# Kernel optimization log

Measured on AMD Instinct MI355X. Metric: run time of the kernel, lower is better.

Reference implementation:

```python
import jax, jax.numpy as jnp
import numpy as np

N, D_IN, D_ATTN = 8192, 48, 8


def setup_inputs() -> dict:
    key = jax.random.key(0)
    ks = jax.random.split(key, 9)
    s = 1.0 / np.sqrt(D_IN)
    return {
        "x": jax.random.normal(ks[0], (N, D_IN), jnp.float32),
        "Kw": jax.random.normal(ks[1], (D_IN, D_ATTN), jnp.float32) * s,
        "Kb": jax.random.normal(ks[2], (D_ATTN,), jnp.float32) * s,
        "Qw": jax.random.normal(ks[3], (D_IN, D_ATTN), jnp.float32) * s,
        "Qb": jax.random.normal(ks[4], (D_ATTN,), jnp.float32) * s,
        "Vw": jax.random.normal(ks[5], (D_IN, D_ATTN), jnp.float32) * s,
        "Vb": jax.random.normal(ks[6], (D_ATTN,), jnp.float32) * s,
        "Zw": jax.random.normal(ks[7], (D_ATTN, D_IN), jnp.float32) * (1.0 / np.sqrt(D_ATTN)),
        "Zb": jax.random.normal(ks[8], (D_IN,), jnp.float32) * (1.0 / np.sqrt(D_ATTN)),
    }


def reference(x, Kw, Kb, Qw, Qb, Vw, Vb, Zw, Zb):
    # Tiny QKV projections: [N,48] -> [N,8]
    Xk = x @ Kw + Kb
    Xq = x @ Qw + Qb
    Xv = x @ Vw + Vb
    # Attention over the batch/row dimension: [N,8]@[8,N] -> [N,N]
    scale = jnp.sqrt(jnp.asarray(D_ATTN, jnp.float32))
    AM = jax.nn.softmax(Xk @ Xq.T / scale, axis=1)  # torch F.softmax 2D default dim=1
    Z = AM @ Xv                                      # [N,8]
    return x + (Z @ Zw + Zb)                         # residual + output proj [N,48]
```

## Files before the change

kernel.cpp:

```cpp
#include <hip/hip_runtime.h>


#define QV_OFF   32768
#define BMAX_OFF 98304
#define PART_OFF 98560

typedef _Float16 f16x2 __attribute__((ext_vector_type(2)));

union HU { unsigned u; f16x2 h; };

static __device__ __forceinline__ unsigned pku(float a, float b) {
    auto v = __builtin_amdgcn_cvt_pkrtz(a, b);
    union { decltype(v) v2; unsigned u; } t;
    t.v2 = v;
    return t.u;
}
static __device__ __forceinline__ f16x2 asH2(unsigned u) {
    HU t; t.u = u; return t.h;
}
static __device__ __forceinline__ float fdot2(f16x2 a, f16x2 b, float c) {
#if __has_builtin(__builtin_amdgcn_fdot2)
    return __builtin_amdgcn_fdot2(a, b, c, false);
#else
    return fmaf((float)a.x, (float)b.x, fmaf((float)a.y, (float)b.y, c));
#endif
}

__global__ __launch_bounds__(256) void proj_kernel(
    const float* __restrict__ x,
    const float* __restrict__ Kw, const float* __restrict__ Kb,
    const float* __restrict__ Qw, const float* __restrict__ Qb,
    const float* __restrict__ Vw, const float* __restrict__ Vb,
    unsigned* __restrict__ Xksf16, unsigned* __restrict__ QV,
    float* __restrict__ bmax)
{
    __shared__ float xs[32 * 49];
    __shared__ float wAll[3 * 388];
    __shared__ float bs[24];
    __shared__ float outv[32][25];
    const int tid = threadIdx.x;
    const int r0 = blockIdx.x * 32;

    for (int i = tid; i < 1536; i += 256) {
        int r = i / 48, c = i - r * 48;
        xs[r * 49 + c] = x[r0 * 48 + i];
    }
    for (int i = tid; i < 384; i += 256) {
        wAll[i]       = Kw[i];
        wAll[388 + i] = Qw[i];
        wAll[776 + i] = Vw[i];
    }
    if (tid < 8)       bs[tid] = Kb[tid];
    else if (tid < 16) bs[tid] = Qb[tid - 8];
    else if (tid < 24) bs[tid] = Vb[tid - 16];
    __syncthreads();

    const int rl = tid >> 3;
    const int g  = tid & 7;
    const int c0 = 3 * g;
    const float* xr = &xs[rl * 49];
    const float* w0 = &wAll[((c0 + 0) >> 3) * 388 + ((c0 + 0) & 7)];
    const float* w1 = &wAll[((c0 + 1) >> 3) * 388 + ((c0 + 1) & 7)];
    const float* w2 = &wAll[((c0 + 2) >> 3) * 388 + ((c0 + 2) & 7)];
    float a0 = bs[c0], a1 = bs[c0 + 1], a2 = bs[c0 + 2];
    #pragma unroll
    for (int k = 0; k < 48; k++) {
        const float xv = xr[k];
        a0 = fmaf(xv, w0[k * 8], a0);
        a1 = fmaf(xv, w1[k * 8], a1);
        a2 = fmaf(xv, w2[k * 8], a2);
    }
    outv[rl][c0] = a0; outv[rl][c0 + 1] = a1; outv[rl][c0 + 2] = a2;
    __syncthreads();

    const float kscale = 0.51008732149f;
    if (tid < 32) {
        uint4 o;
        o.x = pku(outv[tid][0] * kscale, outv[tid][1] * kscale);
        o.y = pku(outv[tid][2] * kscale, outv[tid][3] * kscale);
        o.z = pku(outv[tid][4] * kscale, outv[tid][5] * kscale);
        o.w = pku(outv[tid][6] * kscale, outv[tid][7] * kscale);
        ((uint4*)Xksf16)[r0 + tid] = o;
    } else if (tid < 64) {
        const int r = tid - 32;
        const int j = r0 + r;
        uint4 o;
        o.x = pku(outv[r][8],  outv[r][9]);
        o.y = pku(outv[r][10], outv[r][11]);
        o.z = pku(outv[r][12], outv[r][13]);
        o.w = pku(outv[r][14], outv[r][15]);
        ((uint4*)QV)[(j >> 1) * 4 + (j & 1)] = o;
    } else if (tid < 192) {
        const int t2 = tid - 64;
        const int p = t2 >> 3, c = t2 & 7;
        const int pg = blockIdx.x * 16 + p;
        QV[pg * 16 + 8 + c] = pku(outv[2 * p][16 + c], outv[2 * p + 1][16 + c]);
    } else if (tid < 224) {
        const int r = tid - 192;
        float n2 = 0.f;
        #pragma unroll
        for (int c = 0; c < 8; c++) n2 = fmaf(outv[r][8 + c], outv[r][8 + c], n2);
        #pragma unroll
        for (int off = 16; off > 0; off >>= 1)
            n2 = fmaxf(n2, __shfl_xor(n2, off, 64));
        if (r == 0) bmax[blockIdx.x] = n2;
    }
}

__global__ __launch_bounds__(256) void attn_kernel(
    const unsigned* __restrict__ Xksf16, const unsigned* __restrict__ QV,
    const float* __restrict__ bmax,
    float* __restrict__ part, int P)
{
    __shared__ uint4 tile[256];
    const int tid  = threadIdx.x;
    const int lane = tid & 63;
    const int wv   = tid >> 6;
    const int g    = blockIdx.x & 7;
    const int ch   = blockIdx.x >> 3;

    float m = fmaxf(fmaxf(bmax[lane], bmax[64 + lane]),
                    fmaxf(bmax[128 + lane], bmax[192 + lane]));
    #pragma unroll
    for (int off = 32; off > 0; off >>= 1)
        m = fmaxf(m, __shfl_xor(m, off, 64));
    const float qmax2 = m;

    const int rbase = g * 1024 + wv * 256 + lane;
    f16x2 k2[4][4];
    float sinit[4], l[4], acc[4][8];
    #pragma unroll
    for (int k = 0; k < 4; k++) {
        const uint4 kv = ((const uint4*)Xksf16)[rbase + 64 * k];
        k2[k][0] = asH2(kv.x); k2[k][1] = asH2(kv.y);
        k2[k][2] = asH2(kv.z); k2[k][3] = asH2(kv.w);
        float kn2 = fdot2(k2[k][0], k2[k][0], 0.f);
        kn2 = fdot2(k2[k][1], k2[k][1], kn2);
        kn2 = fdot2(k2[k][2], k2[k][2], kn2);
        kn2 = fdot2(k2[k][3], k2[k][3], kn2);
        sinit[k] = -sqrtf(kn2 * qmax2);
        l[k] = 0.f;
        #pragma unroll
        for (int c = 0; c < 8; c++) acc[k][c] = 0.f;
    }

    const f16x2 one2 = asH2(0x3C003C00u);

    for (int t0 = 0; t0 < P; t0 += 64) {
        const int np = min(64, P - t0);
        __syncthreads();
        for (int i = tid; i < np * 4; i += 256)
            tile[i] = ((const uint4*)QV)[((size_t)ch * P + t0) * 4 + i];
        __syncthreads();

        #pragma unroll 2
        for (int p = 0; p < np; p++) {
            const uint4 qa = tile[p * 4 + 0];
            const uint4 qb = tile[p * 4 + 1];
            const uint4 va = tile[p * 4 + 2];
            const uint4 vb = tile[p * 4 + 3];
            const f16x2 qa0 = asH2(qa.x), qa1 = asH2(qa.y),
                        qa2 = asH2(qa.z), qa3 = asH2(qa.w);
            const f16x2 qb0 = asH2(qb.x), qb1 = asH2(qb.y),
                        qb2 = asH2(qb.z), qb3 = asH2(qb.w);
            #pragma unroll
            for (int k = 0; k < 4; k++) {
                float s0 = fdot2(k2[k][0], qa0, sinit[k]);
                s0 = fdot2(k2[k][1], qa1, s0);
                s0 = fdot2(k2[k][2], qa2, s0);
                s0 = fdot2(k2[k][3], qa3, s0);
                float s1 = fdot2(k2[k][0], qb0, sinit[k]);
                s1 = fdot2(k2[k][1], qb1, s1);
                s1 = fdot2(k2[k][2], qb2, s1);
                s1 = fdot2(k2[k][3], qb3, s1);
                const f16x2 ph = asH2(pku(__builtin_amdgcn_exp2f(s0),
                                          __builtin_amdgcn_exp2f(s1)));
                l[k] = fdot2(ph, one2, l[k]);
                acc[k][0] = fdot2(ph, asH2(va.x), acc[k][0]);
                acc[k][1] = fdot2(ph, asH2(va.y), acc[k][1]);
                acc[k][2] = fdot2(ph, asH2(va.z), acc[k][2]);
                acc[k][3] = fdot2(ph, asH2(va.w), acc[k][3]);
                acc[k][4] = fdot2(ph, asH2(vb.x), acc[k][4]);
                acc[k][5] = fdot2(ph, asH2(vb.y), acc[k][5]);
                acc[k][6] = fdot2(ph, asH2(vb.z), acc[k][6]);
                acc[k][7] = fdot2(ph, asH2(vb.w), acc[k][7]);
            }
        }
    }

    #pragma unroll
    for (int k = 0; k < 4; k++) {
        const int row = rbase + 64 * k;
        #pragma unroll
        for (int c = 0; c < 8; c++)
            part[((size_t)(ch * 9 + c) << 13) + row] = acc[k][c];
        part[((size_t)(ch * 9 + 8) << 13) + row] = l[k];
    }
}

__global__ __launch_bounds__(256) void finish_kernel(
    const float* __restrict__ x,
    const float* __restrict__ Zw, const float* __restrict__ Zb,
    const float* __restrict__ part, float* __restrict__ out, int nch)
{
    __shared__ float red[4][64][10];
    __shared__ float Zs[64][9];
    __shared__ float zw_s[384];
    __shared__ float zb_s[48];
    const int tid = threadIdx.x;
    const int r0 = blockIdx.x * 64;

    for (int i = tid; i < 384; i += 256) zw_s[i] = Zw[i];
    if (tid < 48) zb_s[tid] = Zb[tid];

    const int r = tid & 63, s = tid >> 6;
    const int row = r0 + r;
    const int cps = nch >> 2;
    float a[9];
    #pragma unroll
    for (int c = 0; c < 9; c++) a[c] = 0.f;
    for (int i = 0; i < cps; i++) {
        const int ch = s * cps + i;
        const float* p = part + ((size_t)(ch * 9) << 13) + row;
        #pragma unroll
        for (int c = 0; c < 9; c++) a[c] += p[(size_t)c << 13];
    }
    #pragma unroll
    for (int c = 0; c < 9; c++) red[s][r][c] = a[c];
    __syncthreads();
    if (tid < 64) {
        float b[9];
        #pragma unroll
        for (int c = 0; c < 9; c++)
            b[c] = red[0][tid][c] + red[1][tid][c] + red[2][tid][c] + red[3][tid][c];
        const float inv = 1.0f / b[8];
        #pragma unroll
        for (int c = 0; c < 8; c++) Zs[tid][c] = b[c] * inv;
    }
    __syncthreads();

    for (int e = tid; e < 64 * 48; e += 256) {
        const int rr = e / 48, c = e - rr * 48;
        float o = x[r0 * 48 + e] + zb_s[c];
        #pragma unroll
        for (int k = 0; k < 8; k++) o = fmaf(Zs[rr][k], zw_s[k * 48 + c], o);
        out[r0 * 48 + e] = o;
    }
}

extern "C" void kernel_launch(void* const* d_in, const int* in_sizes, int n_in,
                              void* d_out, int out_size, void* d_ws, size_t ws_size,
                              hipStream_t stream) {
    const float* x  = (const float*)d_in[0];
    const float* Kw = (const float*)d_in[1];
    const float* Kb = (const float*)d_in[2];
    const float* Qw = (const float*)d_in[3];
    const float* Qb = (const float*)d_in[4];
    const float* Vw = (const float*)d_in[5];
    const float* Vb = (const float*)d_in[6];
    const float* Zw = (const float*)d_in[7];
    const float* Zb = (const float*)d_in[8];
    float* out = (float*)d_out;

    float* ws = (float*)d_ws;
    unsigned* Xksf16 = (unsigned*)ws;
    unsigned* QV     = (unsigned*)(ws + QV_OFF);
    float* bmax      = ws + BMAX_OFF;
    float* part      = ws + PART_OFF;

    int nch = 128;
    const size_t avail = ws_size / 4;
    while (nch > 4 && (size_t)PART_OFF + (size_t)nch * 9 * 8192 > avail) nch >>= 1;
    const int P = 4096 / nch;

    proj_kernel<<<256, 256, 0, stream>>>(x, Kw, Kb, Qw, Qb, Vw, Vb,
                                         Xksf16, QV, bmax);
    attn_kernel<<<8 * nch, 256, 0, stream>>>(Xksf16, QV, bmax, part, P);
    finish_kernel<<<128, 256, 0, stream>>>(x, Zw, Zb, part, out, nch);
}
```

Baseline: 134.9 us.

## Switch attention inner loop to packed half2 FMA and store partials in fp16

The attention loop now works on packed half2 values. Each K element is broadcast into both lanes, and one chain of hfma2 computes the scores for two paired rows at once. Score, row-sum and PV accumulation all stay in fp16 instead of going through fdot2 into fp32. The partial sums are written as fp16, which halves the traffic into the finish kernel, and the proj kernel's QV packing is simplified to one store per thread. The aim is higher ALU throughput and less memory traffic. The cost is a large loss of accumulation precision, since the sums cover 32 pairs per chunk and are kept in fp16, which risks error beyond tolerance.

New measurement: 127.5 us. 5.5% less time.

```diff
diff --git a/kernel.cpp b/kernel.cpp
--- a/kernel.cpp
+++ b/kernel.cpp
@@ -1,13 +1,12 @@
 #include <hip/hip_runtime.h>
+#include <hip/hip_fp16.h>
 
 
 #define QV_OFF   32768
 #define BMAX_OFF 98304
 #define PART_OFF 98560
 
-typedef _Float16 f16x2 __attribute__((ext_vector_type(2)));
-
-union HU { unsigned u; f16x2 h; };
+union HU2 { unsigned u; __half2 h; };
 
 static __device__ __forceinline__ unsigned pku(float a, float b) {
     auto v = __builtin_amdgcn_cvt_pkrtz(a, b);
@@ -15,15 +14,8 @@
     t.v2 = v;
     return t.u;
 }
-static __device__ __forceinline__ f16x2 asH2(unsigned u) {
-    HU t; t.u = u; return t.h;
-}
-static __device__ __forceinline__ float fdot2(f16x2 a, f16x2 b, float c) {
-#if __has_builtin(__builtin_amdgcn_fdot2)
-    return __builtin_amdgcn_fdot2(a, b, c, false);
-#else
-    return fmaf((float)a.x, (float)b.x, fmaf((float)a.y, (float)b.y, c));
-#endif
+static __device__ __forceinline__ __half2 asH2(unsigned u) {
+    HU2 t; t.u = u; return t.h;
 }
 
 __global__ __launch_bounds__(256) void proj_kernel(
@@ -73,6 +65,14 @@
     outv[rl][c0] = a0; outv[rl][c0 + 1] = a1; outv[rl][c0 + 2] = a2;
     __syncthreads();
 
+    {
+        const int p = tid >> 4;
+        const int c = (tid >> 1) & 7;
+        const int m = tid & 1;
+        const int col = (m ? 16 : 8) + c;
+        QV[(blockIdx.x * 16 + p) * 16 + m * 8 + c] =
+            pku(outv[2 * p][col], outv[2 * p + 1][col]);
+    }
     const float kscale = 0.51008732149f;
     if (tid < 32) {
         uint4 o;
@@ -81,21 +81,8 @@
         o.z = pku(outv[tid][4] * kscale, outv[tid][5] * kscale);
         o.w = pku(outv[tid][6] * kscale, outv[tid][7] * kscale);
         ((uint4*)Xksf16)[r0 + tid] = o;
-    } else if (tid < 64) {
-        const int r = tid - 32;
-        const int j = r0 + r;
-        uint4 o;
-        o.x = pku(outv[r][8],  outv[r][9]);
-        o.y = pku(outv[r][10], outv[r][11]);
-        o.z = pku(outv[r][12], outv[r][13]);
-        o.w = pku(outv[r][14], outv[r][15]);
-        ((uint4*)QV)[(j >> 1) * 4 + (j & 1)] = o;
-    } else if (tid < 192) {
-        const int t2 = tid - 64;
-        const int p = t2 >> 3, c = t2 & 7;
-        const int pg = blockIdx.x * 16 + p;
-        QV[pg * 16 + 8 + c] = pku(outv[2 * p][16 + c], outv[2 * p + 1][16 + c]);
-    } else if (tid < 224) {
+    }
+    if (tid >= 192 && tid < 224) {
         const int r = tid - 192;
         float n2 = 0.f;
         #pragma unroll
@@ -110,7 +97,7 @@
 __global__ __launch_bounds__(256) void attn_kernel(
     const unsigned* __restrict__ Xksf16, const unsigned* __restrict__ QV,
     const float* __restrict__ bmax,
-    float* __restrict__ part, int P)
+    __half* __restrict__ partH, int P)
 {
     __shared__ uint4 tile[256];
     const int tid  = threadIdx.x;
@@ -127,63 +114,75 @@
     const float qmax2 = m;
 
     const int rbase = g * 1024 + wv * 256 + lane;
-    f16x2 k2[4][4];
-    float sinit[4], l[4], acc[4][8];
+    __half2 k2b[4][8];
+    __half2 sinit2[4], l2[4], acc2[4][8];
+    const __half2 zero2 = __float2half2_rn(0.f);
+    const __half2 one2  = __float2half2_rn(1.f);
     #pragma unroll
     for (int k = 0; k < 4; k++) {
         const uint4 kv = ((const uint4*)Xksf16)[rbase + 64 * k];
-        k2[k][0] = asH2(kv.x); k2[k][1] = asH2(kv.y);
-        k2[k][2] = asH2(kv.z); k2[k][3] = asH2(kv.w);
-        float kn2 = fdot2(k2[k][0], k2[k][0], 0.f);
-        kn2 = fdot2(k2[k][1], k2[k][1], kn2);
-        kn2 = fdot2(k2[k][2], k2[k][2], kn2);
-        kn2 = fdot2(k2[k][3], k2[k][3], kn2);
-        sinit[k] = -sqrtf(kn2 * qmax2);
-        l[k] = 0.f;
-        #pragma unroll
-        for (int c = 0; c < 8; c++) acc[k][c] = 0.f;
-    }
-
-    const f16x2 one2 = asH2(0x3C003C00u);
+        const __half2 k01 = asH2(kv.x), k23 = asH2(kv.y),
+                      k45 = asH2(kv.z), k67 = asH2(kv.w);
+        k2b[k][0] = __low2half2(k01);  k2b[k][1] = __high2half2(k01);
+        k2b[k][2] = __low2half2(k23);  k2b[k][3] = __high2half2(k23);
+        k2b[k][4] = __low2half2(k45);  k2b[k][5] = __high2half2(k45);
+        k2b[k][6] = __low2half2(k67);  k2b[k][7] = __high2half2(k67);
+        float kn2 = 0.f;
+        #pragma unroll
+        for (int c = 0; c < 8; c++) {
+            const float kf = __low2float(k2b[k][c]);
+            kn2 = fmaf(kf, kf, kn2);
+        }
+        sinit2[k] = __float2half2_rn(-sqrtf(kn2 * qmax2));
+        l2[k] = zero2;
+        #pragma unroll
+        for (int c = 0; c < 8; c++) acc2[k][c] = zero2;
+    }
 
     for (int t0 = 0; t0 < P; t0 += 64) {
-        const int np = min(64, P - t0);
+        const int np = (P - t0 < 64) ? (P - t0) : 64;
         __syncthreads();
         for (int i = tid; i < np * 4; i += 256)
             tile[i] = ((const uint4*)QV)[((size_t)ch * P + t0) * 4 + i];
         __syncthreads();
 
-        #pragma unroll 2
+        #pragma unroll 4
         for (int p = 0; p < np; p++) {
-            const uint4 qa = tile[p * 4 + 0];
-            const uint4 qb = tile[p * 4 + 1];
-            const uint4 va = tile[p * 4 + 2];
-            const uint4 vb = tile[p * 4 + 3];
-            const f16x2 qa0 = asH2(qa.x), qa1 = asH2(qa.y),
-                        qa2 = asH2(qa.z), qa3 = asH2(qa.w);
-            const f16x2 qb0 = asH2(qb.x), qb1 = asH2(qb.y),
-                        qb2 = asH2(qb.z), qb3 = asH2(qb.w);
+            const uint4 qp0 = tile[p * 4 + 0];
+            const uint4 qp1 = tile[p * 4 + 1];
+            const uint4 vp0 = tile[p * 4 + 2];
+            const uint4 vp1 = tile[p * 4 + 3];
+            const __half2 q0 = asH2(qp0.x), q1 = asH2(qp0.y),
+                          q2 = asH2(qp0.z), q3 = asH2(qp0.w),
+                          q4 = asH2(qp1.x), q5 = asH2(qp1.y),
+                          q6 = asH2(qp1.z), q7 = asH2(qp1.w);
+            const __half2 v0 = asH2(vp0.x), v1 = asH2(vp0.y),
+                          v2 = asH2(vp0.z), v3 = asH2(vp0.w),
+                          v4 = asH2(vp1.x), v5 = asH2(vp1.y),
+                          v6 = asH2(vp1.z), v7 = asH2(vp1.w);
             #pragma unroll
             for (int k = 0; k < 4; k++) {
-                float s0 = fdot2(k2[k][0], qa0, sinit[k]);
-                s0 = fdot2(k2[k][1], qa1, s0);
-                s0 = fdot2(k2[k][2], qa2, s0);
-                s0 = fdot2(k2[k][3], qa3, s0);
-                float s1 = fdot2(k2[k][0], qb0, sinit[k]);
-                s1 = fdot2(k2[k][1], qb1, s1);
-                s1 = fdot2(k2[k][2], qb2, s1);
-                s1 = fdot2(k2[k][3], qb3, s1);
-                const f16x2 ph = asH2(pku(__builtin_amdgcn_exp2f(s0),
-                                          __builtin_amdgcn_exp2f(s1)));
-                l[k] = fdot2(ph, one2, l[k]);
-                acc[k][0] = fdot2(ph, asH2(va.x), acc[k][0]);
-                acc[k][1] = fdot2(ph, asH2(va.y), acc[k][1]);
-                acc[k][2] = fdot2(ph, asH2(va.z), acc[k][2]);
-                acc[k][3] = fdot2(ph, asH2(va.w), acc[k][3]);
-                acc[k][4] = fdot2(ph, asH2(vb.x), acc[k][4]);
-                acc[k][5] = fdot2(ph, asH2(vb.y), acc[k][5]);
-                acc[k][6] = fdot2(ph, asH2(vb.z), acc[k][6]);
-                acc[k][7] = fdot2(ph, asH2(vb.w), acc[k][7]);
+                __half2 s2 = sinit2[k];
+                s2 = __hfma2(k2b[k][0], q0, s2);
+                s2 = __hfma2(k2b[k][1], q1, s2);
+                s2 = __hfma2(k2b[k][2], q2, s2);
+                s2 = __hfma2(k2b[k][3], q3, s2);
+                s2 = __hfma2(k2b[k][4], q4, s2);
+                s2 = __hfma2(k2b[k][5], q5, s2);
+                s2 = __hfma2(k2b[k][6], q6, s2);
+                s2 = __hfma2(k2b[k][7], q7, s2);
+                const float p0 = __builtin_amdgcn_exp2f(__low2float(s2));
+                const float p1 = __builtin_amdgcn_exp2f(__high2float(s2));
+                const __half2 ph = asH2(pku(p0, p1));
+                l2[k] = __hfma2(ph, one2, l2[k]);
+                acc2[k][0] = __hfma2(ph, v0, acc2[k][0]);
+                acc2[k][1] = __hfma2(ph, v1, acc2[k][1]);
+                acc2[k][2] = __hfma2(ph, v2, acc2[k][2]);
+                acc2[k][3] = __hfma2(ph, v3, acc2[k][3]);
+                acc2[k][4] = __hfma2(ph, v4, acc2[k][4]);
+                acc2[k][5] = __hfma2(ph, v5, acc2[k][5]);
+                acc2[k][6] = __hfma2(ph, v6, acc2[k][6]);
+                acc2[k][7] = __hfma2(ph, v7, acc2[k][7]);
             }
         }
     }
@@ -192,16 +191,19 @@
     for (int k = 0; k < 4; k++) {
         const int row = rbase + 64 * k;
         #pragma unroll
-        for (int c = 0; c < 8; c++)
-            part[((size_t)(ch * 9 + c) << 13) + row] = acc[k][c];
-        part[((size_t)(ch * 9 + 8) << 13) + row] = l[k];
+        for (int c = 0; c < 8; c++) {
+            const float af = __low2float(acc2[k][c]) + __high2float(acc2[k][c]);
+            partH[((size_t)(ch * 9 + c) << 13) + row] = __float2half_rn(af);
+        }
+        const float lf = __low2float(l2[k]) + __high2float(l2[k]);
+        partH[((size_t)(ch * 9 + 8) << 13) + row] = __float2half_rn(lf);
     }
 }
 
 __global__ __launch_bounds__(256) void finish_kernel(
     const float* __restrict__ x,
     const float* __restrict__ Zw, const float* __restrict__ Zb,
-    const float* __restrict__ part, float* __restrict__ out, int nch)
+    const __half* __restrict__ partH, float* __restrict__ out, int nch)
 {
     __shared__ float red[4][64][10];
     __shared__ float Zs[64][9];
@@ -221,9 +223,9 @@
     for (int c = 0; c < 9; c++) a[c] = 0.f;
     for (int i = 0; i < cps; i++) {
         const int ch = s * cps + i;
-        const float* p = part + ((size_t)(ch * 9) << 13) + row;
-        #pragma unroll
-        for (int c = 0; c < 9; c++) a[c] += p[(size_t)c << 13];
+        const __half* p = partH + ((size_t)(ch * 9) << 13) + row;
+        #pragma unroll
+        for (int c = 0; c < 9; c++) a[c] += __half2float(p[(size_t)c << 13]);
     }
     #pragma unroll
     for (int c = 0; c < 9; c++) red[s][r][c] = a[c];
@@ -266,15 +268,15 @@
     unsigned* Xksf16 = (unsigned*)ws;
     unsigned* QV     = (unsigned*)(ws + QV_OFF);
     float* bmax      = ws + BMAX_OFF;
-    float* part      = ws + PART_OFF;
+    __half* partH    = (__half*)(ws + PART_OFF);
 
     int nch = 128;
-    const size_t avail = ws_size / 4;
-    while (nch > 4 && (size_t)PART_OFF + (size_t)nch * 9 * 8192 > avail) nch >>= 1;
+    while (nch > 4 &&
+           (size_t)PART_OFF * 4 + (size_t)nch * 9 * 8192 * 2 > ws_size) nch >>= 1;
     const int P = 4096 / nch;
 
     proj_kernel<<<256, 256, 0, stream>>>(x, Kw, Kb, Qw, Qb, Vw, Vb,
                                          Xksf16, QV, bmax);
-    attn_kernel<<<8 * nch, 256, 0, stream>>>(Xksf16, QV, bmax, part, P);
-    finish_kernel<<<128, 256, 0, stream>>>(x, Zw, Zb, part, out, nch);
-}
+    attn_kernel<<<8 * nch, 256, 0, stream>>>(Xksf16, QV, bmax, partH, P);
+    finish_kernel<<<128, 256, 0, stream>>>(x, Zw, Zb, partH, out, nch);
+}
```
